# Optimization experiments

Hardware: AMD Instinct MI355X
Metric: run time of the kernel (lower is better)

## Reference

```python
import jax, jax.numpy as jnp
import numpy as np

N = 100000   # nodes
E = 1600000  # edges (avg degree 16)
DIN = 64
H = 64
OUT = 64


def _lin(key, fan_out, fan_in):
    s = 1.0 / np.sqrt(fan_in)
    return jax.random.uniform(key, (fan_out, fan_in), jnp.float32, -s, s)


def setup_inputs() -> dict:
    key = jax.random.key(0)
    ks = jax.random.split(key, 32)
    inp = {
        "x": jax.random.normal(ks[0], (N, DIN), jnp.float32),
        "edge_index": jax.random.randint(ks[1], (2, E), 0, N, dtype=jnp.int32),
    }
    dims = [(H, DIN), (H, H), (OUT, H)]  # (out_dim, in_dim) per layer
    for li, (do, di) in enumerate(dims):
        k = jax.random.split(ks[2 + li], 5)
        inp[f"Wl{li}"] = _lin(k[0], do, di)            # lin_l weight (on aggregated neighbors)
        inp[f"bl{li}"] = jnp.zeros((do,), jnp.float32)  # lin_l bias
        inp[f"Wr{li}"] = _lin(k[1], do, di)            # lin_r (root), no bias in PyG
        inp[f"Ws{li}"] = _lin(k[2], do, di)            # skip Linear weight
        inp[f"bs{li}"] = jnp.zeros((do,), jnp.float32)  # skip Linear bias
    return inp


def _sage_skip_layer(h, src, dst, Wl, bl, Wr, Ws, bs):
    # max-aggregate neighbor (source) features at each destination node
    agg = jax.ops.segment_max(h[src], dst, num_segments=N)  # [N, d_in]
    agg = jnp.where(jnp.isfinite(agg), agg, 0.0)            # empty segments -> 0 (PyG fill)
    conv = agg @ Wl.T + bl + h @ Wr.T                        # SAGEConv output
    skip = h @ Ws.T + bs                                     # parallel Linear
    return jax.nn.relu(conv + skip)


def reference(x, edge_index, Wl0, bl0, Wr0, Ws0, bs0,
              Wl1, bl1, Wr1, Ws1, bs1,
              Wl2, bl2, Wr2, Ws2, bs2):
    src, dst = edge_index[0], edge_index[1]
    h = _sage_skip_layer(x, src, dst, Wl0, bl0, Wr0, Ws0, bs0)
    h = _sage_skip_layer(h, src, dst, Wl1, bl1, Wr1, Ws1, bs1)
    h = _sage_skip_layer(h, src, dst, Wl2, bl2, Wr2, Ws2, bs2)
    return h
```

## Files before the change

### kernel.cpp

```cpp
#include <hip/hip_runtime.h>
#include <hip/hip_bf16.h>
#include <math.h>

#define FEAT 64
#define BKT_SHIFT 9
#define NB_PAD 256
#define PART_GRID 256
#define SRC_BITS 17

typedef __attribute__((ext_vector_type(8))) short short8;
typedef __attribute__((ext_vector_type(4))) float f32x4;

__device__ __forceinline__ float bf_lo(unsigned u) { return __uint_as_float(u << 16); }
__device__ __forceinline__ float bf_hi(unsigned u) { return __uint_as_float(u & 0xFFFF0000u); }
__device__ __forceinline__ unsigned short f2bf(float f) {
    unsigned b = __float_as_uint(f);
    return (unsigned short)((b + 0x7FFFu + ((b >> 16) & 1u)) >> 16);
}
__device__ __forceinline__ unsigned pack_exact(float lo, float hi) {
    return (__float_as_uint(lo) >> 16) | (__float_as_uint(hi) & 0xFFFF0000u);
}

__global__ __launch_bounds__(256) void hist_kernel(const int* __restrict__ dst,
                                                   int* __restrict__ bktCnt, int nE) {
    __shared__ int hist[NB_PAD];
    int t = threadIdx.x;
    hist[t] = 0;
    __syncthreads();
    int chunk = ((nE + PART_GRID - 1) / PART_GRID + 1) & ~1;
    int begin = blockIdx.x * chunk;
    int end = begin + chunk; if (end > nE) end = nE;
    for (int i = begin + 2 * t; i < end; i += 512) {
        if (i + 1 < end) {
            int2 d2 = *(const int2*)&dst[i];
            atomicAdd(&hist[d2.x >> BKT_SHIFT], 1);
            atomicAdd(&hist[d2.y >> BKT_SHIFT], 1);
        } else {
            atomicAdd(&hist[dst[i] >> BKT_SHIFT], 1);
        }
    }
    __syncthreads();
    if (hist[t]) atomicAdd(&bktCnt[t], hist[t]);
}

__global__ __launch_bounds__(256) void bucket_scan_kernel(const int* __restrict__ bktCnt,
                                                          int* __restrict__ baseC,
                                                          int* __restrict__ baseP,
                                                          int* __restrict__ bktCursor) {
    __shared__ int wsum[4];
    int t = threadIdx.x;
    int own = bktCnt[t];
    int lane = t & 63, w = t >> 6;
    int inc = own;
    for (int d = 1; d < 64; d <<= 1) { int tt = __shfl_up(inc, d); if (lane >= d) inc += tt; }
    if (lane == 63) wsum[w] = inc;
    __syncthreads();
    if (t == 0) { int r = 0; for (int k = 0; k < 4; ++k) { int v = wsum[k]; wsum[k] = r; r += v; } }
    __syncthreads();
    int excl = (inc - own) + wsum[w];
    baseC[t] = excl;
    int pb = (excl + 16 * t + 15) & ~15;
    baseP[t] = pb;
    bktCursor[t] = pb;
}

__global__ __launch_bounds__(256) void partition_kernel(const int* __restrict__ src,
                                                        const int* __restrict__ dst,
                                                        int* __restrict__ bktCursor,
                                                        unsigned* __restrict__ pairs, int nE) {
    __shared__ int hist[NB_PAD];
    __shared__ int lofs[NB_PAD];
    int t = threadIdx.x;
    hist[t] = 0;
    __syncthreads();
    int chunk = ((nE + PART_GRID - 1) / PART_GRID + 1) & ~1;
    int begin = blockIdx.x * chunk;
    int end = begin + chunk; if (end > nE) end = nE;
    for (int i = begin + 2 * t; i < end; i += 512) {
        if (i + 1 < end) {
            int2 d2 = *(const int2*)&dst[i];
            atomicAdd(&hist[d2.x >> BKT_SHIFT], 1);
            atomicAdd(&hist[d2.y >> BKT_SHIFT], 1);
        } else {
            atomicAdd(&hist[dst[i] >> BKT_SHIFT], 1);
        }
    }
    __syncthreads();
    int c = hist[t];
    lofs[t] = c ? atomicAdd(&bktCursor[t], c) : 0;
    __syncthreads();
    const unsigned LMASK = (1u << BKT_SHIFT) - 1u;
    for (int i = begin + 2 * t; i < end; i += 512) {
        if (i + 1 < end) {
            int2 d2 = *(const int2*)&dst[i];
            int2 s2 = *(const int2*)&src[i];
            int p0 = atomicAdd(&lofs[d2.x >> BKT_SHIFT], 1);
            pairs[p0] = (((unsigned)d2.x & LMASK) << SRC_BITS) | (unsigned)s2.x;
            int p1 = atomicAdd(&lofs[d2.y >> BKT_SHIFT], 1);
            pairs[p1] = (((unsigned)d2.y & LMASK) << SRC_BITS) | (unsigned)s2.y;
        } else {
            int d = dst[i];
            int pos = atomicAdd(&lofs[d >> BKT_SHIFT], 1);
            pairs[pos] = (((unsigned)d & LMASK) << SRC_BITS) | (unsigned)src[i];
        }
    }
}

__global__ __launch_bounds__(512) void csr_bucket_kernel(const unsigned* __restrict__ pairs,
                                                         const int* __restrict__ baseP,
                                                         const int* __restrict__ baseC,
                                                         const int* __restrict__ bktCnt,
                                                         int* __restrict__ off,
                                                         int* __restrict__ csr,
                                                         int N, int E) {
    __shared__ int deg[512];
    __shared__ int cur[512];
    __shared__ int wsum[8];
    int b = blockIdx.x;
    int t = threadIdx.x;
    int lo = b << BKT_SHIFT;
    int nloc = N - lo; if (nloc > 512) nloc = 512;
    int e0p = baseP[b];
    int e0c = baseC[b];
    int cnt = bktCnt[b];
    deg[t] = 0;
    __syncthreads();
    for (int e = t; e < cnt; e += 512)
        atomicAdd(&deg[pairs[e0p + e] >> SRC_BITS], 1);
    __syncthreads();
    int v = deg[t];
    int lane = t & 63, w = t >> 6;
    int inc = v;
    for (int d = 1; d < 64; d <<= 1) { int tt = __shfl_up(inc, d); if (lane >= d) inc += tt; }
    if (lane == 63) wsum[w] = inc;
    __syncthreads();
    if (t == 0) { int r = 0; for (int k = 0; k < 8; ++k) { int x = wsum[k]; wsum[k] = r; r += x; } }
    __syncthreads();
    int excl = (inc - v) + wsum[w];
    if (t < nloc) off[lo + t] = e0c + excl;
    cur[t] = excl;
    if (b == 0 && t == 0) off[N] = E;
    __syncthreads();
    for (int e = t; e < cnt; e += 512) {
        unsigned p = pairs[e0p + e];
        int pos = atomicAdd(&cur[p >> SRC_BITS], 1);
        csr[e0c + pos] = (int)(p & ((1u << SRC_BITS) - 1));
    }
}

__global__ void prep_kernel(const float* __restrict__ Wl0, const float* __restrict__ Wr0,
                            const float* __restrict__ Ws0, const float* __restrict__ bl0,
                            const float* __restrict__ bs0,
                            const float* __restrict__ Wl1, const float* __restrict__ Wr1,
                            const float* __restrict__ Ws1, const float* __restrict__ bl1,
                            const float* __restrict__ bs1,
                            const float* __restrict__ Wl2, const float* __restrict__ Wr2,
                            const float* __restrict__ Ws2, const float* __restrict__ bl2,
                            const float* __restrict__ bs2,
                            unsigned short* __restrict__ wlb,
                            unsigned short* __restrict__ wcb,
                            float* __restrict__ bias) {
    int i = blockIdx.x * blockDim.x + threadIdx.x;
    if (i < 3 * FEAT * FEAT) {
        int li = i >> 12, j = i & 4095;
        const float* Wl = (li == 0) ? Wl0 : (li == 1) ? Wl1 : Wl2;
        const float* Wr = (li == 0) ? Wr0 : (li == 1) ? Wr1 : Wr2;
        const float* Ws = (li == 0) ? Ws0 : (li == 1) ? Ws1 : Ws2;
        wlb[i] = f2bf(Wl[j]);
        wcb[i] = f2bf(Wr[j] + Ws[j]);
    }
    if (i < 3 * FEAT) {
        int li = i >> 6, j = i & 63;
        const float* bl = (li == 0) ? bl0 : (li == 1) ? bl1 : bl2;
        const float* bs = (li == 0) ? bs0 : (li == 1) ? bs1 : bs2;
        bias[i] = bl[j] + bs[j];
    }
}

__global__ __launch_bounds__(256) void conv_kernel(const float* __restrict__ in,
                                                   unsigned short* __restrict__ outb,
                                                   int nElem) {
    int base = (blockIdx.x * blockDim.x + threadIdx.x) * 8;
    if (base >= nElem) return;
    float4 a = *(const float4*)(in + base);
    float4 b = *(const float4*)(in + base + 4);
    ushort4 p0 = {f2bf(a.x), f2bf(a.y), f2bf(a.z), f2bf(a.w)};
    ushort4 p1 = {f2bf(b.x), f2bf(b.y), f2bf(b.z), f2bf(b.w)};
    *(ushort4*)(outb + base) = p0;
    *(ushort4*)(outb + base + 4) = p1;
}

__global__ __launch_bounds__(256) void agg_kernel(const unsigned short* __restrict__ hb,
                                                  const int* __restrict__ off,
                                                  const int* __restrict__ csr_src,
                                                  unsigned short* __restrict__ ab,
                                                  int nNodes) {
    int gid = blockIdx.x * blockDim.x + threadIdx.x;
    int n = gid >> 3;
    int q = gid & 7;
    if (n >= nNodes) return;

    int e0 = off[n], e1 = off[n + 1];
    const float NEG = -INFINITY;
    float acc[8] = {NEG, NEG, NEG, NEG, NEG, NEG, NEG, NEG};

    int e = e0;
    for (; e + 4 <= e1; e += 4) {
        int s0 = csr_src[e], s1 = csr_src[e + 1], s2 = csr_src[e + 2], s3 = csr_src[e + 3];
        uint4 v0 = *(const uint4*)&hb[(size_t)s0 * FEAT + q * 8];
        uint4 v1 = *(const uint4*)&hb[(size_t)s1 * FEAT + q * 8];
        uint4 v2 = *(const uint4*)&hb[(size_t)s2 * FEAT + q * 8];
        uint4 v3 = *(const uint4*)&hb[(size_t)s3 * FEAT + q * 8];
#define ACCUM(v)                                            \
        acc[0] = fmaxf(acc[0], bf_lo(v.x)); acc[1] = fmaxf(acc[1], bf_hi(v.x)); \
        acc[2] = fmaxf(acc[2], bf_lo(v.y)); acc[3] = fmaxf(acc[3], bf_hi(v.y)); \
        acc[4] = fmaxf(acc[4], bf_lo(v.z)); acc[5] = fmaxf(acc[5], bf_hi(v.z)); \
        acc[6] = fmaxf(acc[6], bf_lo(v.w)); acc[7] = fmaxf(acc[7], bf_hi(v.w));
        ACCUM(v0) ACCUM(v1) ACCUM(v2) ACCUM(v3)
    }
    for (; e < e1; ++e) {
        int s0 = csr_src[e];
        uint4 v0 = *(const uint4*)&hb[(size_t)s0 * FEAT + q * 8];
        ACCUM(v0)
    }
#undef ACCUM

    uint4 outv;
    if (e1 > e0) {
        outv.x = pack_exact(acc[0], acc[1]);
        outv.y = pack_exact(acc[2], acc[3]);
        outv.z = pack_exact(acc[4], acc[5]);
        outv.w = pack_exact(acc[6], acc[7]);
    } else {
        outv = make_uint4(0, 0, 0, 0);
    }
    *(uint4*)&ab[(size_t)n * FEAT + q * 8] = outv;
}

template <bool BF16OUT>
__global__ __launch_bounds__(256) void transform_mfma_kernel(
        const unsigned short* __restrict__ hb,
        const unsigned short* __restrict__ ab,
        const unsigned short* __restrict__ Wlb,
        const unsigned short* __restrict__ Wcb,
        const float* __restrict__ bias,
        float* __restrict__ outf,
        unsigned short* __restrict__ outb,
        int nNodes, int tpb, int nTiles) {
    int wave = threadIdx.x >> 6;
    int lane = threadIdx.x & 63;
    int f0 = wave << 4;
    int lm = lane & 15;
    int lk = lane >> 4;

    short8 aWl0 = *(const short8*)&Wlb[(f0 + lm) * FEAT + lk * 8];
    short8 aWl1 = *(const short8*)&Wlb[(f0 + lm) * FEAT + lk * 8 + 32];
    short8 aWc0 = *(const short8*)&Wcb[(f0 + lm) * FEAT + lk * 8];
    short8 aWc1 = *(const short8*)&Wcb[(f0 + lm) * FEAT + lk * 8 + 32];
    f32x4 b4 = *(const f32x4*)&bias[f0 + lk * 4];

    int t0 = blockIdx.x * tpb;
    int t1 = t0 + tpb; if (t1 > nTiles) t1 = nTiles;
#pragma unroll 2
    for (int t = t0; t < t1; ++t) {
        int nb = t << 4;
        int n = nb + lm;
        int nr = (n < nNodes) ? n : (nNodes - 1);
        const unsigned short* __restrict__ ar = ab + (size_t)nr * FEAT;
        const unsigned short* __restrict__ hr = hb + (size_t)nr * FEAT;
        short8 bA0 = *(const short8*)(ar + lk * 8);
        short8 bA1 = *(const short8*)(ar + lk * 8 + 32);
        short8 bH0 = *(const short8*)(hr + lk * 8);
        short8 bH1 = *(const short8*)(hr + lk * 8 + 32);

        f32x4 acc = {0.f, 0.f, 0.f, 0.f};
        acc = __builtin_amdgcn_mfma_f32_16x16x32_bf16(aWl0, bA0, acc, 0, 0, 0);
        acc = __builtin_amdgcn_mfma_f32_16x16x32_bf16(aWl1, bA1, acc, 0, 0, 0);
        acc = __builtin_amdgcn_mfma_f32_16x16x32_bf16(aWc0, bH0, acc, 0, 0, 0);
        acc = __builtin_amdgcn_mfma_f32_16x16x32_bf16(aWc1, bH1, acc, 0, 0, 0);

        if (n < nNodes) {
            float v0 = fmaxf(acc[0] + b4[0], 0.f);
            float v1 = fmaxf(acc[1] + b4[1], 0.f);
            float v2 = fmaxf(acc[2] + b4[2], 0.f);
            float v3 = fmaxf(acc[3] + b4[3], 0.f);
            if (BF16OUT) {
                ushort4 p = {f2bf(v0), f2bf(v1), f2bf(v2), f2bf(v3)};
                *(ushort4*)&outb[(size_t)n * FEAT + f0 + lk * 4] = p;
            } else {
                float4 p = make_float4(v0, v1, v2, v3);
                *(float4*)&outf[(size_t)n * FEAT + f0 + lk * 4] = p;
            }
        }
    }
}

extern "C" void kernel_launch(void* const* d_in, const int* in_sizes, int n_in,
                              void* d_out, int out_size, void* d_ws, size_t ws_size,
                              hipStream_t stream) {
    const float* x   = (const float*)d_in[0];
    const int* eidx  = (const int*)d_in[1];
    const int N  = in_sizes[0] / FEAT;
    const int E  = in_sizes[1] / 2;
    const int* src = eidx;
    const int* dst = eidx + E;

    const float* Wl[3]; const float* bl[3]; const float* Wr[3];
    const float* Ws[3]; const float* bs[3];
    for (int li = 0; li < 3; ++li) {
        Wl[li] = (const float*)d_in[2 + 5 * li + 0];
        bl[li] = (const float*)d_in[2 + 5 * li + 1];
        Wr[li] = (const float*)d_in[2 + 5 * li + 2];
        Ws[li] = (const float*)d_in[2 + 5 * li + 3];
        bs[li] = (const float*)d_in[2 + 5 * li + 4];
    }

    auto align256 = [](size_t v) { return (v + 255) & ~(size_t)255; };
    char* ws = (char*)d_ws;
    int* off       = (int*)ws;  ws += align256((size_t)(N + 1) * 4);
    int* bktCnt    = (int*)ws;  ws += align256(NB_PAD * 4);
    int* baseC     = (int*)ws;  ws += align256((NB_PAD + 1) * 4);
    int* baseP     = (int*)ws;  ws += align256((NB_PAD + 1) * 4);
    int* bktCursor = (int*)ws;  ws += align256(NB_PAD * 4);
    unsigned* pairs = (unsigned*)ws; ws += align256(((size_t)E + 16 * NB_PAD + 64) * 4);
    int* csr_src   = (int*)ws;  ws += align256((size_t)E * 4);
    unsigned short* wlb = (unsigned short*)ws; ws += align256(3 * FEAT * FEAT * 2);
    unsigned short* wcb = (unsigned short*)ws; ws += align256(3 * FEAT * FEAT * 2);
    float* biasbuf = (float*)ws; ws += align256(3 * FEAT * 4);
    unsigned short* xb  = (unsigned short*)ws; ws += align256((size_t)N * FEAT * 2);
    unsigned short* ab  = (unsigned short*)ws; ws += align256((size_t)N * FEAT * 2);
    unsigned short* h1b = (unsigned short*)ws; ws += align256((size_t)N * FEAT * 2);
    unsigned short* h2b = (unsigned short*)ws; ws += align256((size_t)N * FEAT * 2);

    const int TB = 256;
    int nBkt = (N + (1 << BKT_SHIFT) - 1) >> BKT_SHIFT;

    hipMemsetAsync(bktCnt, 0, NB_PAD * 4, stream);
    hist_kernel<<<PART_GRID, TB, 0, stream>>>(dst, bktCnt, E);
    bucket_scan_kernel<<<1, TB, 0, stream>>>(bktCnt, baseC, baseP, bktCursor);
    partition_kernel<<<PART_GRID, TB, 0, stream>>>(src, dst, bktCursor, pairs, E);
    csr_bucket_kernel<<<nBkt, 512, 0, stream>>>(pairs, baseP, baseC, bktCnt, off, csr_src, N, E);

    prep_kernel<<<(3 * FEAT * FEAT + TB - 1) / TB, TB, 0, stream>>>(
        Wl[0], Wr[0], Ws[0], bl[0], bs[0],
        Wl[1], Wr[1], Ws[1], bl[1], bs[1],
        Wl[2], Wr[2], Ws[2], bl[2], bs[2], wlb, wcb, biasbuf);
    int convBlocks = (N * FEAT / 8 + TB - 1) / TB;
    conv_kernel<<<convBlocks, TB, 0, stream>>>(x, xb, N * FEAT);

    int aggBlocks = (N * 8 + TB - 1) / TB;
    int nTiles16 = (N + 15) / 16;
    const int TPB = 4;
    int trfBlocks = (nTiles16 + TPB - 1) / TPB;

    agg_kernel<<<aggBlocks, TB, 0, stream>>>(xb, off, csr_src, ab, N);
    transform_mfma_kernel<true><<<trfBlocks, TB, 0, stream>>>(
        xb, ab, wlb + 0 * 4096, wcb + 0 * 4096, biasbuf + 0 * 64, nullptr, h1b, N, TPB, nTiles16);
    agg_kernel<<<aggBlocks, TB, 0, stream>>>(h1b, off, csr_src, ab, N);
    transform_mfma_kernel<true><<<trfBlocks, TB, 0, stream>>>(
        h1b, ab, wlb + 1 * 4096, wcb + 1 * 4096, biasbuf + 1 * 64, nullptr, h2b, N, TPB, nTiles16);
    agg_kernel<<<aggBlocks, TB, 0, stream>>>(h2b, off, csr_src, ab, N);
    transform_mfma_kernel<false><<<trfBlocks, TB, 0, stream>>>(
        h2b, ab, wlb + 2 * 4096, wcb + 2 * 4096, biasbuf + 2 * 64, (float*)d_out, nullptr, N, TPB, nTiles16);
}
```

Baseline: 208.0 us.

## Fuse max-aggregation and MFMA transform into one per-layer kernel via LDS

Merges the gather/max aggregation kernel and the MFMA linear transform kernel into a single kernel per layer. Each 256-thread block aggregates 64 nodes into a swizzled LDS tile, synchronises, then runs the MFMA transform reading aggregated features from LDS instead of a global buffer. This removes the global write and re-read of the aggregate array and three kernel launches. In exchange each block now ends its gather phase at a barrier before the transform, and the LDS tile may reduce occupancy.

```diff
diff --git a/kernel.cpp b/kernel.cpp
--- a/kernel.cpp
+++ b/kernel.cpp
@@ -190,68 +190,67 @@
     *(ushort4*)(outb + base + 4) = p1;
 }
 
-__global__ __launch_bounds__(256) void agg_kernel(const unsigned short* __restrict__ hb,
-                                                  const int* __restrict__ off,
-                                                  const int* __restrict__ csr_src,
-                                                  unsigned short* __restrict__ ab,
-                                                  int nNodes) {
-    int gid = blockIdx.x * blockDim.x + threadIdx.x;
-    int n = gid >> 3;
-    int q = gid & 7;
-    if (n >= nNodes) return;
-
-    int e0 = off[n], e1 = off[n + 1];
-    const float NEG = -INFINITY;
-    float acc[8] = {NEG, NEG, NEG, NEG, NEG, NEG, NEG, NEG};
-
-    int e = e0;
-    for (; e + 4 <= e1; e += 4) {
-        int s0 = csr_src[e], s1 = csr_src[e + 1], s2 = csr_src[e + 2], s3 = csr_src[e + 3];
-        uint4 v0 = *(const uint4*)&hb[(size_t)s0 * FEAT + q * 8];
-        uint4 v1 = *(const uint4*)&hb[(size_t)s1 * FEAT + q * 8];
-        uint4 v2 = *(const uint4*)&hb[(size_t)s2 * FEAT + q * 8];
-        uint4 v3 = *(const uint4*)&hb[(size_t)s3 * FEAT + q * 8];
-#define ACCUM(v)                                            \
-        acc[0] = fmaxf(acc[0], bf_lo(v.x)); acc[1] = fmaxf(acc[1], bf_hi(v.x)); \
-        acc[2] = fmaxf(acc[2], bf_lo(v.y)); acc[3] = fmaxf(acc[3], bf_hi(v.y)); \
-        acc[4] = fmaxf(acc[4], bf_lo(v.z)); acc[5] = fmaxf(acc[5], bf_hi(v.z)); \
-        acc[6] = fmaxf(acc[6], bf_lo(v.w)); acc[7] = fmaxf(acc[7], bf_hi(v.w));
-        ACCUM(v0) ACCUM(v1) ACCUM(v2) ACCUM(v3)
-    }
-    for (; e < e1; ++e) {
-        int s0 = csr_src[e];
-        uint4 v0 = *(const uint4*)&hb[(size_t)s0 * FEAT + q * 8];
-        ACCUM(v0)
-    }
-#undef ACCUM
-
-    uint4 outv;
-    if (e1 > e0) {
-        outv.x = pack_exact(acc[0], acc[1]);
-        outv.y = pack_exact(acc[2], acc[3]);
-        outv.z = pack_exact(acc[4], acc[5]);
-        outv.w = pack_exact(acc[6], acc[7]);
-    } else {
-        outv = make_uint4(0, 0, 0, 0);
-    }
-    *(uint4*)&ab[(size_t)n * FEAT + q * 8] = outv;
-}
-
 template <bool BF16OUT>
-__global__ __launch_bounds__(256) void transform_mfma_kernel(
+__global__ __launch_bounds__(256) void fused_layer_kernel(
         const unsigned short* __restrict__ hb,
-        const unsigned short* __restrict__ ab,
+        const int* __restrict__ off,
+        const int* __restrict__ csr_src,
         const unsigned short* __restrict__ Wlb,
         const unsigned short* __restrict__ Wcb,
         const float* __restrict__ bias,
         float* __restrict__ outf,
         unsigned short* __restrict__ outb,
-        int nNodes, int tpb, int nTiles) {
-    int wave = threadIdx.x >> 6;
-    int lane = threadIdx.x & 63;
-    int f0 = wave << 4;
-    int lm = lane & 15;
-    int lk = lane >> 4;
+        int nNodes) {
+    __shared__ __align__(16) unsigned short agg_s[64 * FEAT];
+
+    int t = threadIdx.x;
+    int nb0 = blockIdx.x * 64;
+
+    int g = t >> 3;
+    int q = t & 7;
+#pragma unroll
+    for (int rep = 0; rep < 2; ++rep) {
+        int nl = rep * 32 + g;
+        int n = nb0 + nl;
+        uint4 outv = make_uint4(0, 0, 0, 0);
+        if (n < nNodes) {
+            int e0 = off[n], e1 = off[n + 1];
+            if (e1 > e0) {
+                const float NEG = -INFINITY;
+                float acc[8] = {NEG, NEG, NEG, NEG, NEG, NEG, NEG, NEG};
+#define ACCUM(v)                                                            \
+                acc[0] = fmaxf(acc[0], bf_lo(v.x)); acc[1] = fmaxf(acc[1], bf_hi(v.x)); \
+                acc[2] = fmaxf(acc[2], bf_lo(v.y)); acc[3] = fmaxf(acc[3], bf_hi(v.y)); \
+                acc[4] = fmaxf(acc[4], bf_lo(v.z)); acc[5] = fmaxf(acc[5], bf_hi(v.z)); \
+                acc[6] = fmaxf(acc[6], bf_lo(v.w)); acc[7] = fmaxf(acc[7], bf_hi(v.w));
+                int e = e0;
+                for (; e + 4 <= e1; e += 4) {
+                    int s0 = csr_src[e],     s1 = csr_src[e + 1];
+                    int s2 = csr_src[e + 2], s3 = csr_src[e + 3];
+                    uint4 v0 = *(const uint4*)&hb[(size_t)s0 * FEAT + q * 8];
+                    uint4 v1 = *(const uint4*)&hb[(size_t)s1 * FEAT + q * 8];
+                    uint4 v2 = *(const uint4*)&hb[(size_t)s2 * FEAT + q * 8];
+                    uint4 v3 = *(const uint4*)&hb[(size_t)s3 * FEAT + q * 8];
+                    ACCUM(v0) ACCUM(v1) ACCUM(v2) ACCUM(v3)
+                }
+                for (; e < e1; ++e) {
+                    int s0 = csr_src[e];
+                    uint4 v0 = *(const uint4*)&hb[(size_t)s0 * FEAT + q * 8];
+                    ACCUM(v0)
+                }
+#undef ACCUM
+                outv.x = pack_exact(acc[0], acc[1]);
+                outv.y = pack_exact(acc[2], acc[3]);
+                outv.z = pack_exact(acc[4], acc[5]);
+                outv.w = pack_exact(acc[6], acc[7]);
+            }
+        }
+        *(uint4*)&agg_s[nl * FEAT + ((q ^ (nl & 7)) << 3)] = outv;
+    }
+    __syncthreads();
+
+    int wave = t >> 6, lane = t & 63;
+    int f0 = wave << 4, lm = lane & 15, lk = lane >> 4;
 
     short8 aWl0 = *(const short8*)&Wlb[(f0 + lm) * FEAT + lk * 8];
     short8 aWl1 = *(const short8*)&Wlb[(f0 + lm) * FEAT + lk * 8 + 32];
@@ -259,17 +258,14 @@
     short8 aWc1 = *(const short8*)&Wcb[(f0 + lm) * FEAT + lk * 8 + 32];
     f32x4 b4 = *(const f32x4*)&bias[f0 + lk * 4];
 
-    int t0 = blockIdx.x * tpb;
-    int t1 = t0 + tpb; if (t1 > nTiles) t1 = nTiles;
-#pragma unroll 2
-    for (int t = t0; t < t1; ++t) {
-        int nb = t << 4;
-        int n = nb + lm;
+#pragma unroll
+    for (int tile = 0; tile < 4; ++tile) {
+        int nl = tile * 16 + lm;
+        int n = nb0 + nl;
         int nr = (n < nNodes) ? n : (nNodes - 1);
-        const unsigned short* __restrict__ ar = ab + (size_t)nr * FEAT;
         const unsigned short* __restrict__ hr = hb + (size_t)nr * FEAT;
-        short8 bA0 = *(const short8*)(ar + lk * 8);
-        short8 bA1 = *(const short8*)(ar + lk * 8 + 32);
+        short8 bA0 = *(const short8*)&agg_s[nl * FEAT + (((lk)     ^ (nl & 7)) << 3)];
+        short8 bA1 = *(const short8*)&agg_s[nl * FEAT + (((lk + 4) ^ (nl & 7)) << 3)];
         short8 bH0 = *(const short8*)(hr + lk * 8);
         short8 bH1 = *(const short8*)(hr + lk * 8 + 32);
 
@@ -328,7 +324,6 @@
     unsigned short* wcb = (unsigned short*)ws; ws += align256(3 * FEAT * FEAT * 2);
     float* biasbuf = (float*)ws; ws += align256(3 * FEAT * 4);
     unsigned short* xb  = (unsigned short*)ws; ws += align256((size_t)N * FEAT * 2);
-    unsigned short* ab  = (unsigned short*)ws; ws += align256((size_t)N * FEAT * 2);
     unsigned short* h1b = (unsigned short*)ws; ws += align256((size_t)N * FEAT * 2);
     unsigned short* h2b = (unsigned short*)ws; ws += align256((size_t)N * FEAT * 2);
 
@@ -348,18 +343,15 @@
     int convBlocks = (N * FEAT / 8 + TB - 1) / TB;
     conv_kernel<<<convBlocks, TB, 0, stream>>>(x, xb, N * FEAT);
 
-    int aggBlocks = (N * 8 + TB - 1) / TB;
-    int nTiles16 = (N + 15) / 16;
-    const int TPB = 4;
-    int trfBlocks = (nTiles16 + TPB - 1) / TPB;
-
-    agg_kernel<<<aggBlocks, TB, 0, stream>>>(xb, off, csr_src, ab, N);
-    transform_mfma_kernel<true><<<trfBlocks, TB, 0, stream>>>(
-        xb, ab, wlb + 0 * 4096, wcb + 0 * 4096, biasbuf + 0 * 64, nullptr, h1b, N, TPB, nTiles16);
-    agg_kernel<<<aggBlocks, TB, 0, stream>>>(h1b, off, csr_src, ab, N);
-    transform_mfma_kernel<true><<<trfBlocks, TB, 0, stream>>>(
-        h1b, ab, wlb + 1 * 4096, wcb + 1 * 4096, biasbuf + 1 * 64, nullptr, h2b, N, TPB, nTiles16);
-    agg_kernel<<<aggBlocks, TB, 0, stream>>>(h2b, off, csr_src, ab, N);
-    transform_mfma_kernel<false><<<trfBlocks, TB, 0, stream>>>(
-        h2b, ab, wlb + 2 * 4096, wcb + 2 * 4096, biasbuf + 2 * 64, (float*)d_out, nullptr, N, TPB, nTiles16);
-}
+    int fusedBlocks = (N + 63) / 64;
+
+    fused_layer_kernel<true><<<fusedBlocks, TB, 0, stream>>>(
+        xb, off, csr_src, wlb + 0 * 4096, wcb + 0 * 4096, biasbuf + 0 * 64,
+        nullptr, h1b, N);
+    fused_layer_kernel<true><<<fusedBlocks, TB, 0, stream>>>(
+        h1b, off, csr_src, wlb + 1 * 4096, wcb + 1 * 4096, biasbuf + 1 * 64,
+        nullptr, h2b, N);
+    fused_layer_kernel<false><<<fusedBlocks, TB, 0, stream>>>(
+        h2b, off, csr_src, wlb + 2 * 4096, wcb + 2 * 4096, biasbuf + 2 * 64,
+        (float*)d_out, nullptr, N);
+}
```

Result: faster. 177.5 us (-14.7%).
